# Optimization experiments

Measured on AMD Instinct MI355X. Metric: run time of the kernel, lower is better.

## Reference

```python
import jax, jax.numpy as jnp
import numpy as np

B, HID, REC, NC, T = 512, 196, 488, 35, 120
BN_EPS = 1e-3


def _bn(x, g, b):
    # eval-mode CustomBatchNorm1d: running_mean=0, running_var=1
    return g * (x / jnp.sqrt(1.0 + BN_EPS)) + b


def _gru(x, Wih, Whh, bih, bhh):
    """Standard torch nn.GRU (batch_first), h0 = 0. x: [B,T,D] -> [B,T,H]."""
    H = Whh.shape[1]
    def step(h, xt):
        xg = xt @ Wih.T + bih          # [B,3H]
        hg = h @ Whh.T + bhh           # [B,3H]
        xr, xz, xn = jnp.split(xg, 3, axis=1)
        hr, hz, hn = jnp.split(hg, 3, axis=1)
        r = jax.nn.sigmoid(xr + hr)
        z = jax.nn.sigmoid(xz + hz)
        n = jnp.tanh(xn + r * hn)
        h2 = (1.0 - z) * n + z * h
        return h2, h2
    h0 = jnp.zeros((x.shape[0], H), x.dtype)
    _, ys = jax.lax.scan(step, h0, jnp.swapaxes(x, 0, 1))
    return jnp.swapaxes(ys, 0, 1)


def _custom_gru(x, Wih, Whh, bih):
    """CustomGRUCell (eval mode: prev_target=0 so weight_tf term vanishes)."""
    H = Whh.shape[1]
    Whh_rz = Whh[:2 * H]
    Whh_n = Whh[2 * H:]
    b_r, b_z, b_n = bih[:H], bih[H:2 * H], bih[2 * H:]
    def step(h, xt):
        xg = xt @ Wih.T                 # [B,3H], no bias in F.linear
        xr, xz, xn = jnp.split(xg, 3, axis=1)
        hg = h @ Whh_rz.T               # only r,z rows needed (h_h chunk unused)
        hr, hz = jnp.split(hg, 2, axis=1)
        r = jax.nn.sigmoid(xr + hr + b_r)
        u = jax.nn.sigmoid(xz + hz + b_z)
        n = jax.nn.softmax(xn + (r * h) @ Whh_n.T + b_n, axis=1)
        h2 = (1.0 - u) * n + u * h
        return h2, h2
    h0 = jnp.zeros((x.shape[0], H), x.dtype)
    _, ys = jax.lax.scan(step, h0, jnp.swapaxes(x, 0, 1))
    return jnp.swapaxes(ys, 0, 1)


def setup_inputs() -> dict:
    key = jax.random.key(0)
    ks = jax.random.split(key, 16)
    s = 0.05
    inp = {
        "z_in": jax.random.normal(ks[0], (B, HID), jnp.float32),
        "W0": jax.random.normal(ks[1], (HID, HID), jnp.float32) * s,
        "b0": jnp.zeros((HID,), jnp.float32),
        "g0": jnp.full((1, HID), 0.1, jnp.float32),
        "beta0": jnp.zeros((1, HID), jnp.float32),
        "W1": jax.random.normal(ks[2], (HID, HID), jnp.float32) * s,
        "b1": jnp.zeros((HID,), jnp.float32),
        "g1": jnp.full((1, HID), 0.1, jnp.float32),
        "beta1": jnp.zeros((1, HID), jnp.float32),
        "gru0_Wih": jax.random.normal(ks[3], (3 * REC, HID), jnp.float32) * s,
        "gru0_Whh": jax.random.normal(ks[4], (3 * REC, REC), jnp.float32) * s,
        "gru0_bih": jax.random.normal(ks[5], (3 * REC,), jnp.float32) * s,
        "gru0_bhh": jax.random.normal(ks[6], (3 * REC,), jnp.float32) * s,
        "gru1_Wih": jax.random.normal(ks[7], (3 * REC, REC), jnp.float32) * s,
        "gru1_Whh": jax.random.normal(ks[8], (3 * REC, REC), jnp.float32) * s,
        "gru1_bih": jax.random.normal(ks[9], (3 * REC,), jnp.float32) * s,
        "gru1_bhh": jax.random.normal(ks[10], (3 * REC,), jnp.float32) * s,
        "cell_Wih": jax.random.normal(ks[11], (3 * NC, REC), jnp.float32) * s,
        "cell_Whh": jax.random.normal(ks[12], (3 * NC, NC), jnp.float32) * s,
        "cell_bih": jax.random.normal(ks[13], (3 * NC,), jnp.float32) * s,
    }
    return inp


def reference(z_in, W0, b0, g0, beta0, W1, b1, g1, beta1,
              gru0_Wih, gru0_Whh, gru0_bih, gru0_bhh,
              gru1_Wih, gru1_Whh, gru1_bih, gru1_bhh,
              cell_Wih, cell_Whh, cell_bih):
    z = _bn(z_in @ W0.T + b0, g0, beta0)
    z = _bn(z @ W1.T + b1, g1, beta1)
    z_reps = jnp.broadcast_to(z[:, None, :], (z.shape[0], T, z.shape[1]))
    x = _gru(z_reps, gru0_Wih, gru0_Whh, gru0_bih, gru0_bhh)
    x = _gru(x, gru1_Wih, gru1_Whh, gru1_bih, gru1_bhh)
    x_out = _custom_gru(x, cell_Wih, cell_Whh, cell_bih)  # [B,T,NCHARS]
    return x_out
```

## Files before the change

### kernel.cpp

```cpp
#include <hip/hip_runtime.h>
#include <math.h>

#define Bsz 512
#define HID 196
#define REC 488
#define NC  35
#define TT  120
#define G3  1464
#define NSLOT 123

#define KT   8
#define NCH  61
#define NB   61
#define CELLB 32
#define NGRID (3*NB + CELLB)
#define WSL  (NCH*KT*24)

struct CellSmem { float xs[16][492]; float hs[16][36]; float rh[16][36]; };

__device__ __forceinline__ float sigmoidf_(float x) { return 1.0f / (1.0f + __expf(-x)); }

__device__ __forceinline__ void gbar(int* bar, int target) {
  __syncthreads();
  if (threadIdx.x == 0) {
    __builtin_amdgcn_fence(__ATOMIC_RELEASE, "agent");
    __hip_atomic_fetch_add(bar, 1, __ATOMIC_RELAXED, __HIP_MEMORY_SCOPE_AGENT);
    while (__hip_atomic_load(bar, __ATOMIC_RELAXED, __HIP_MEMORY_SCOPE_AGENT) < target)
      __builtin_amdgcn_s_sleep(2);
    __builtin_amdgcn_fence(__ATOMIC_ACQUIRE, "agent");
  }
  __syncthreads();
}

__global__ void dense_bn_kernel(const float* __restrict__ X, const float* __restrict__ W,
                                const float* __restrict__ bias, const float* __restrict__ g,
                                const float* __restrict__ beta, float* __restrict__ Y) {
  __shared__ float xs[HID];
  int b = blockIdx.x;
  for (int k = threadIdx.x; k < HID; k += blockDim.x) xs[k] = X[(size_t)b*HID + k];
  __syncthreads();
  int j = threadIdx.x;
  if (j < HID) {
    const float4* wr = (const float4*)(W + (size_t)j*HID);
    float acc = 0.f;
    #pragma unroll 7
    for (int k4 = 0; k4 < HID/4; ++k4) {
      float4 w4 = wr[k4];
      acc += xs[4*k4+0]*w4.x + xs[4*k4+1]*w4.y + xs[4*k4+2]*w4.z + xs[4*k4+3]*w4.w;
    }
    float v = (acc + bias[j]) * 0.9995003746f;
    Y[(size_t)b*HID + j] = g[j]*v + beta[j];
  }
}

__global__ __launch_bounds__(256)
void xg0v2_kernel(const float* __restrict__ Z, const float* __restrict__ Wih,
                  const float* __restrict__ bih, float* __restrict__ XGT) {
  __shared__ float zs[HID*4];
  int b0 = blockIdx.x << 2;
  for (int idx = threadIdx.x; idx < HID*4; idx += 256) {
    int k = idx >> 2, i = idx & 3;
    zs[idx] = Z[(size_t)(b0+i)*HID + k];
  }
  __syncthreads();
  for (int c = threadIdx.x; c < G3; c += 256) {
    const float4* wr = (const float4*)(Wih + (size_t)c*HID);
    float a0=0.f,a1=0.f,a2=0.f,a3=0.f;
    for (int k4 = 0; k4 < HID/4; ++k4) {
      float4 w = wr[k4];
      const float* zp = zs + (k4<<4);
      a0=fmaf(w.x,zp[0],a0);  a1=fmaf(w.x,zp[1],a1);  a2=fmaf(w.x,zp[2],a2);  a3=fmaf(w.x,zp[3],a3);
      a0=fmaf(w.y,zp[4],a0);  a1=fmaf(w.y,zp[5],a1);  a2=fmaf(w.y,zp[6],a2);  a3=fmaf(w.y,zp[7],a3);
      a0=fmaf(w.z,zp[8],a0);  a1=fmaf(w.z,zp[9],a1);  a2=fmaf(w.z,zp[10],a2); a3=fmaf(w.z,zp[11],a3);
      a0=fmaf(w.w,zp[12],a0); a1=fmaf(w.w,zp[13],a1); a2=fmaf(w.w,zp[14],a2); a3=fmaf(w.w,zp[15],a3);
    }
    float bb = bih[c];
    XGT[(size_t)c*Bsz + b0+0] = a0 + bb;
    XGT[(size_t)c*Bsz + b0+1] = a1 + bb;
    XGT[(size_t)c*Bsz + b0+2] = a2 + bb;
    XGT[(size_t)c*Bsz + b0+3] = a3 + bb;
  }
}

__global__ __launch_bounds__(256)
void wtrans_kernel(const float* __restrict__ Whh0, const float* __restrict__ Wih1,
                   const float* __restrict__ Whh1, float* __restrict__ Wt2) {
  int blk = blockIdx.x;
  int stage = blk / NB, j = blk - stage*NB;
  const float* Wsrc = (stage==0) ? Whh0 : (stage==1) ? Wih1 : Whh1;
  float* dst = Wt2 + (size_t)blk*WSL;
  for (int idx = threadIdx.x; idx < WSL; idx += 256) {
    int ck = idx / 192, rem = idx - ck*192;
    int k = rem / 24, r = rem - k*24;
    int g = r >> 3, cl = r & 7;
    dst[idx] = Wsrc[(size_t)(g*REC + j*8 + cl)*REC + ck*8 + k];
  }
}

__device__ __forceinline__ void gemm24s(const float* __restrict__ AT, int b,
                                        const float* __restrict__ wp,
                                        float (&acc)[24])
{
  float av[KT], nv[KT];
  #pragma unroll
  for (int k = 0; k < KT; ++k) av[k] = AT[(size_t)k*Bsz + b];
  for (int ck = 0; ck < NCH; ++ck) {
    if (ck + 1 < NCH) {
      const float* src = AT + (size_t)(ck+1)*KT*Bsz + b;
      #pragma unroll
      for (int k = 0; k < KT; ++k) nv[k] = src[(size_t)k*Bsz];
    }
    const float* w = wp + ck*192;
    #pragma unroll
    for (int k = 0; k < KT; ++k) {
      float a = av[k];
      #pragma unroll
      for (int r = 0; r < 24; ++r)
        acc[r] = fmaf(a, w[k*24 + r], acc[r]);
    }
    #pragma unroll
    for (int k = 0; k < KT; ++k) av[k] = nv[k];
  }
}

__global__ __launch_bounds__(512)
void pers_kernel(const float* __restrict__ xg0T,
                 float* __restrict__ h0T, float* __restrict__ h1T,
                 float* __restrict__ xg1T, float* __restrict__ hc,
                 float* __restrict__ out,
                 const float* __restrict__ Wt2,
                 const float* __restrict__ bhh0,
                 const float* __restrict__ bih1, const float* __restrict__ bhh1,
                 const float* __restrict__ cWih, const float* __restrict__ cWhh,
                 const float* __restrict__ cb, int* __restrict__ bar)
{
  __shared__ CellSmem S;
  const int blk = blockIdx.x;
  const int tid = threadIdx.x;
  const int stage = (blk < NB) ? 0 : (blk < 2*NB) ? 1 : (blk < 3*NB) ? 2 : 3;
  const int l = tid & 63, w = tid >> 6;
  const float* wslice = Wt2 + (size_t)blk*WSL;

  for (int s = 0; s < NSLOT; ++s) {
    if (stage == 0) {
      if (s < TT) {
        int j = blk;
        const float* hprevT = h0T + (size_t)((s+1)&1)*REC*Bsz;
        float*       hnewT  = h0T + (size_t)(s&1)*REC*Bsz;
        float acc[24] = {0};
        gemm24s(hprevT, tid, wslice, acc);
        int b = tid, c0 = j*8;
        #pragma unroll
        for (int cl = 0; cl < 8; ++cl) {
          int c = c0 + cl;
          float xrv = xg0T[(size_t)c*Bsz + b];
          float xzv = xg0T[(size_t)(REC+c)*Bsz + b];
          float xnv = xg0T[(size_t)(2*REC+c)*Bsz + b];
          float r = sigmoidf_(xrv + acc[cl]      + bhh0[c]);
          float z = sigmoidf_(xzv + acc[8+cl]    + bhh0[REC+c]);
          float n = tanhf   (xnv + r*(acc[16+cl] + bhh0[2*REC+c]));
          hnewT[(size_t)c*Bsz + b] = (1.f-z)*n + z*hprevT[(size_t)c*Bsz + b];
        }
      }
    } else if (stage == 1) {
      if (s >= 1 && s <= TT) {
        int t1 = s - 1;
        const float* xT   = h0T  + (size_t)(t1&1)*REC*Bsz;
        float*       xgwT = xg1T + (size_t)(t1&1)*G3*Bsz;
        float acc[24] = {0};
        gemm24s(xT, tid, wslice, acc);
        int b = tid, c0 = (blk - NB)*8;
        #pragma unroll
        for (int cl = 0; cl < 8; ++cl) {
          int c = c0 + cl;
          xgwT[(size_t)c*Bsz + b]         = acc[cl];
          xgwT[(size_t)(REC+c)*Bsz + b]   = acc[8+cl];
          xgwT[(size_t)(2*REC+c)*Bsz + b] = acc[16+cl];
        }
      }
    } else if (stage == 2) {
      if (s >= 2 && s <= TT+1) {
        int t2 = s - 2;
        const float* hprevT = h1T  + (size_t)((t2+1)&1)*REC*Bsz;
        float*       hnewT  = h1T  + (size_t)(t2&1)*REC*Bsz;
        const float* xgrT   = xg1T + (size_t)(t2&1)*G3*Bsz;
        float acc[24] = {0};
        gemm24s(hprevT, tid, wslice, acc);
        int b = tid, c0 = (blk - 2*NB)*8;
        #pragma unroll
        for (int cl = 0; cl < 8; ++cl) {
          int c = c0 + cl;
          float xrv = xgrT[(size_t)c*Bsz + b];
          float xzv = xgrT[(size_t)(REC+c)*Bsz + b];
          float xnv = xgrT[(size_t)(2*REC+c)*Bsz + b];
          float r = sigmoidf_(xrv + acc[cl]   + bih1[c]     + bhh1[c]);
          float z = sigmoidf_(xzv + acc[8+cl] + bih1[REC+c] + bhh1[REC+c]);
          float n = tanhf   (xnv + bih1[2*REC+c] + r*(acc[16+cl] + bhh1[2*REC+c]));
          hnewT[(size_t)c*Bsz + b] = (1.f-z)*n + z*hprevT[(size_t)c*Bsz + b];
        }
      }
    } else {
      if (s >= 3) {
        int t3 = s - 3;
        int b0 = (blk - 3*NB) << 4;
        const float* xT = h1T + (size_t)(t3&1)*REC*Bsz;
        const float* hp = hc  + (size_t)((t3+1)&1)*Bsz*NC;
        float*       hn = hc  + (size_t)(t3&1)*Bsz*NC;
        for (int idx = tid; idx < 16*REC; idx += 512) {
          int k = idx >> 4, it = idx & 15;
          S.xs[it][k] = xT[(size_t)k*Bsz + b0 + it];
        }
        if (l < NC) {
          #pragma unroll
          for (int q = 0; q < 2; ++q) {
            int it = (w<<1) + q;
            S.hs[it][l] = hp[(size_t)(b0+it)*NC + l];
          }
        }
        __syncthreads();
        for (int q = 0; q < 2; ++q) {
          int it = (w<<1) + q;
          int b = b0 + it;
          float v = -1e30f, u = 0.f, hpc = 0.f;
          if (l < NC) {
            const float4* wr4 = (const float4*)(cWih + (size_t)l*REC);
            const float4* wz4 = (const float4*)(cWih + (size_t)(NC+l)*REC);
            const float4* wn4 = (const float4*)(cWih + (size_t)(2*NC+l)*REC);
            const float4* xs4 = (const float4*)(S.xs[it]);
            float xr=0.f, xz=0.f, xn=0.f;
            #pragma unroll 2
            for (int k4 = 0; k4 < REC/4; ++k4) {
              float4 xv = xs4[k4];
              float4 wa = wr4[k4], wb = wz4[k4], wc = wn4[k4];
              xr += wa.x*xv.x + wa.y*xv.y + wa.z*xv.z + wa.w*xv.w;
              xz += wb.x*xv.x + wb.y*xv.y + wb.z*xv.z + wb.w*xv.w;
              xn += wc.x*xv.x + wc.y*xv.y + wc.z*xv.z + wc.w*xv.w;
            }
            float hr=0.f, hz=0.f;
            for (int k = 0; k < NC; ++k) {
              float hv = S.hs[it][k];
              hr = fmaf(hv, cWhh[(size_t)l*NC + k], hr);
              hz = fmaf(hv, cWhh[(size_t)(NC+l)*NC + k], hz);
            }
            float r = sigmoidf_(xr + hr + cb[l]);
            u       = sigmoidf_(xz + hz + cb[NC+l]);
            hpc = S.hs[it][l];
            S.rh[it][l] = r * hpc;
            v = xn;
          }
          __syncthreads();
          if (l < NC) {
            float hnn = 0.f;
            for (int k = 0; k < NC; ++k)
              hnn = fmaf(S.rh[it][k], cWhh[(size_t)(2*NC+l)*NC + k], hnn);
            v = v + hnn + cb[2*NC+l];
          }
          float m = v;
          #pragma unroll
          for (int o = 32; o; o >>= 1) m = fmaxf(m, __shfl_xor(m, o));
          float e = (l < NC) ? __expf(v - m) : 0.f;
          float ss = e;
          #pragma unroll
          for (int o = 32; o; o >>= 1) ss += __shfl_xor(ss, o);
          if (l < NC) {
            float h2 = (1.f - u)*(e/ss) + u*hpc;
            hn[(size_t)b*NC + l] = h2;
            out[((size_t)b*TT + t3)*NC + l] = h2;
          }
          __syncthreads();
        }
      }
    }
    gbar(bar, NGRID*(s+1));
  }
}

extern "C" void kernel_launch(void* const* d_in, const int* in_sizes, int n_in,
                              void* d_out, int out_size, void* d_ws, size_t ws_size,
                              hipStream_t stream) {
  const float* z_in  = (const float*)d_in[0];
  const float* W0    = (const float*)d_in[1];
  const float* b0    = (const float*)d_in[2];
  const float* g0    = (const float*)d_in[3];
  const float* beta0 = (const float*)d_in[4];
  const float* W1    = (const float*)d_in[5];
  const float* b1    = (const float*)d_in[6];
  const float* g1    = (const float*)d_in[7];
  const float* beta1 = (const float*)d_in[8];
  const float* Wih0  = (const float*)d_in[9];
  const float* Whh0  = (const float*)d_in[10];
  const float* bih0  = (const float*)d_in[11];
  const float* bhh0  = (const float*)d_in[12];
  const float* Wih1  = (const float*)d_in[13];
  const float* Whh1  = (const float*)d_in[14];
  const float* bih1  = (const float*)d_in[15];
  const float* bhh1  = (const float*)d_in[16];
  const float* cWih  = (const float*)d_in[17];
  const float* cWhh  = (const float*)d_in[18];
  const float* cbih  = (const float*)d_in[19];
  float* out = (float*)d_out;

  float* ws   = (float*)d_ws;
  int*   bar  = (int*)ws;
  float* h0T  = ws   + 256;
  float* h1T  = h0T  + 2*(size_t)REC*Bsz;
  float* hcb  = h1T  + 2*(size_t)REC*Bsz;
  float* xg1T = hcb  + 2*(size_t)Bsz*NC;
  float* xg0T = xg1T + 2*(size_t)G3*Bsz;
  float* z1   = xg0T + (size_t)G3*Bsz;
  float* z2   = z1   + (size_t)Bsz*HID;
  float* Wt2  = z2   + (size_t)Bsz*HID;

  size_t zero_floats = 256 + 4*(size_t)REC*Bsz + 2*(size_t)Bsz*NC;
  hipMemsetAsync(ws, 0, zero_floats*sizeof(float), stream);

  dense_bn_kernel<<<Bsz, 256, 0, stream>>>(z_in, W0, b0, g0, beta0, z1);
  dense_bn_kernel<<<Bsz, 256, 0, stream>>>(z1,   W1, b1, g1, beta1, z2);
  xg0v2_kernel   <<<128, 256, 0, stream>>>(z2, Wih0, bih0, xg0T);
  wtrans_kernel  <<<3*NB, 256, 0, stream>>>(Whh0, Wih1, Whh1, Wt2);

  pers_kernel<<<NGRID, 512, 0, stream>>>(xg0T, h0T, h1T, xg1T, hcb, out,
                                         Wt2, bhh0, bih1, bhh1, cWih, cWhh, cbih, bar);
}
```

Baseline: 11.84 ms.

## Use relaxed agent-scope atomic loads/stores and workgroup fences in grid barrier

Cross-block shared activations (hidden states, gate pre-activations) are now read and written with relaxed agent-scope atomic loads and stores. This lets the grid barrier use workgroup-scope fences instead of agent-scope fences, avoiding the cost of full cache writeback and invalidate at every step. The GEMM activation prefetch also moves from double buffering to a three-buffer rotation so more loads are in flight. The risk is memory-model correctness if any cross-block data path is still read with plain loads, and atomic loads may be slower than normal cached loads.

```diff
diff --git a/kernel.cpp b/kernel.cpp
--- a/kernel.cpp
+++ b/kernel.cpp
@@ -20,14 +20,21 @@
 
 __device__ __forceinline__ float sigmoidf_(float x) { return 1.0f / (1.0f + __expf(-x)); }
 
+__device__ __forceinline__ float ldc(const float* p) {
+  return __hip_atomic_load(p, __ATOMIC_RELAXED, __HIP_MEMORY_SCOPE_AGENT);
+}
+__device__ __forceinline__ void stc(float* p, float v) {
+  __hip_atomic_store(p, v, __ATOMIC_RELAXED, __HIP_MEMORY_SCOPE_AGENT);
+}
+
 __device__ __forceinline__ void gbar(int* bar, int target) {
   __syncthreads();
   if (threadIdx.x == 0) {
-    __builtin_amdgcn_fence(__ATOMIC_RELEASE, "agent");
+    __builtin_amdgcn_fence(__ATOMIC_RELEASE, "workgroup");
     __hip_atomic_fetch_add(bar, 1, __ATOMIC_RELAXED, __HIP_MEMORY_SCOPE_AGENT);
     while (__hip_atomic_load(bar, __ATOMIC_RELAXED, __HIP_MEMORY_SCOPE_AGENT) < target)
       __builtin_amdgcn_s_sleep(2);
-    __builtin_amdgcn_fence(__ATOMIC_ACQUIRE, "agent");
+    __builtin_amdgcn_fence(__ATOMIC_ACQUIRE, "workgroup");
   }
   __syncthreads();
 }
@@ -101,26 +108,36 @@
                                         const float* __restrict__ wp,
                                         float (&acc)[24])
 {
-  float av[KT], nv[KT];
-  #pragma unroll
-  for (int k = 0; k < KT; ++k) av[k] = AT[(size_t)k*Bsz + b];
-  for (int ck = 0; ck < NCH; ++ck) {
-    if (ck + 1 < NCH) {
-      const float* src = AT + (size_t)(ck+1)*KT*Bsz + b;
-      #pragma unroll
-      for (int k = 0; k < KT; ++k) nv[k] = src[(size_t)k*Bsz];
-    }
-    const float* w = wp + ck*192;
+  const float* base = AT + b;
+  float bufA[KT], bufB[KT], bufC[KT];
+
+  auto pf = [&](float (&buf)[KT], int c) {
+    const float* src = base + (size_t)c*KT*Bsz;
+    #pragma unroll
+    for (int k = 0; k < KT; ++k) buf[k] = ldc(src + (size_t)k*Bsz);
+  };
+  auto fm = [&](const float (&buf)[KT], int c) {
+    const float* w = wp + c*192;
     #pragma unroll
     for (int k = 0; k < KT; ++k) {
-      float a = av[k];
+      float a = buf[k];
       #pragma unroll
       for (int r = 0; r < 24; ++r)
         acc[r] = fmaf(a, w[k*24 + r], acc[r]);
     }
-    #pragma unroll
-    for (int k = 0; k < KT; ++k) av[k] = nv[k];
-  }
+  };
+
+  pf(bufA, 0);
+  pf(bufB, 1);
+  for (int ck = 0; ck < NCH-1; ck += 3) {
+    pf(bufC, ck+2);
+    fm(bufA, ck);
+    pf(bufA, (ck+3 < NCH) ? ck+3 : NCH-1);
+    fm(bufB, ck+1);
+    pf(bufB, (ck+4 < NCH) ? ck+4 : NCH-1);
+    fm(bufC, ck+2);
+  }
+  fm(bufA, NCH-1);
 }
 
 __global__ __launch_bounds__(512)
@@ -159,7 +176,8 @@
           float r = sigmoidf_(xrv + acc[cl]      + bhh0[c]);
           float z = sigmoidf_(xzv + acc[8+cl]    + bhh0[REC+c]);
           float n = tanhf   (xnv + r*(acc[16+cl] + bhh0[2*REC+c]));
-          hnewT[(size_t)c*Bsz + b] = (1.f-z)*n + z*hprevT[(size_t)c*Bsz + b];
+          float hp = ldc(hprevT + (size_t)c*Bsz + b);
+          stc(hnewT + (size_t)c*Bsz + b, (1.f-z)*n + z*hp);
         }
       }
     } else if (stage == 1) {
@@ -173,9 +191,9 @@
         #pragma unroll
         for (int cl = 0; cl < 8; ++cl) {
           int c = c0 + cl;
-          xgwT[(size_t)c*Bsz + b]         = acc[cl];
-          xgwT[(size_t)(REC+c)*Bsz + b]   = acc[8+cl];
-          xgwT[(size_t)(2*REC+c)*Bsz + b] = acc[16+cl];
+          stc(xgwT + (size_t)c*Bsz + b,         acc[cl]);
+          stc(xgwT + (size_t)(REC+c)*Bsz + b,   acc[8+cl]);
+          stc(xgwT + (size_t)(2*REC+c)*Bsz + b, acc[16+cl]);
         }
       }
     } else if (stage == 2) {
@@ -190,13 +208,14 @@
         #pragma unroll
         for (int cl = 0; cl < 8; ++cl) {
           int c = c0 + cl;
-          float xrv = xgrT[(size_t)c*Bsz + b];
-          float xzv = xgrT[(size_t)(REC+c)*Bsz + b];
-          float xnv = xgrT[(size_t)(2*REC+c)*Bsz + b];
+          float xrv = ldc(xgrT + (size_t)c*Bsz + b);
+          float xzv = ldc(xgrT + (size_t)(REC+c)*Bsz + b);
+          float xnv = ldc(xgrT + (size_t)(2*REC+c)*Bsz + b);
           float r = sigmoidf_(xrv + acc[cl]   + bih1[c]     + bhh1[c]);
           float z = sigmoidf_(xzv + acc[8+cl] + bih1[REC+c] + bhh1[REC+c]);
           float n = tanhf   (xnv + bih1[2*REC+c] + r*(acc[16+cl] + bhh1[2*REC+c]));
-          hnewT[(size_t)c*Bsz + b] = (1.f-z)*n + z*hprevT[(size_t)c*Bsz + b];
+          float hp = ldc(hprevT + (size_t)c*Bsz + b);
+          stc(hnewT + (size_t)c*Bsz + b, (1.f-z)*n + z*hp);
         }
       }
     } else {
@@ -208,7 +227,7 @@
         float*       hn = hc  + (size_t)(t3&1)*Bsz*NC;
         for (int idx = tid; idx < 16*REC; idx += 512) {
           int k = idx >> 4, it = idx & 15;
-          S.xs[it][k] = xT[(size_t)k*Bsz + b0 + it];
+          S.xs[it][k] = ldc(xT + (size_t)k*Bsz + b0 + it);
         }
         if (l < NC) {
           #pragma unroll
```

Result: slower. 14.51 ms (+22.6%).
